# Optimization experiments

Hardware: AMD Instinct MI355X
Metric: run time of the kernel (lower is better)

Reference implementation:

```python
import jax, jax.numpy as jnp
import numpy as np

N, IN_C, HID, H1, E, EP = 4096, 256, 128, 4, 131072, 131072
TH, TL, FF = 4, 2, 512  # transformer heads, layers, ffn dim
D = HID  # transformer d_model


def setup_inputs() -> dict:
    key = jax.random.key(0)
    ks = jax.random.split(key, 32)
    s = 0.05
    inp = {
        'features': jax.random.normal(ks[0], (N, IN_C), jnp.float32),
        'src': jax.random.randint(ks[1], (E,), 0, N),
        'dst': jax.random.randint(ks[2], (E,), 0, N),
        'psrc': jax.random.randint(ks[3], (EP,), 0, N),
        'pdst': jax.random.randint(ks[4], (EP,), 0, N),
        # GAT layer 1: in=256 -> heads=4, out=128
        'W1': jax.random.normal(ks[5], (H1 * HID, IN_C), jnp.float32) * s,
        'al1': jax.random.normal(ks[6], (H1, HID), jnp.float32) * s,
        'ar1': jax.random.normal(ks[7], (H1, HID), jnp.float32) * s,
        'b1': jnp.zeros((H1 * HID,), jnp.float32),
        # GAT layer 2: in=512 -> heads=1, out=128
        'W2': jax.random.normal(ks[8], (HID, H1 * HID), jnp.float32) * s,
        'al2': jax.random.normal(ks[9], (1, HID), jnp.float32) * s,
        'ar2': jax.random.normal(ks[10], (1, HID), jnp.float32) * s,
        'b2': jnp.zeros((HID,), jnp.float32),
        # Transformer encoder (TL layers, torch TransformerEncoderLayer post-norm, relu)
        'tw_qkv': jax.random.normal(ks[11], (TL, 3 * D, D), jnp.float32) * s,
        'tb_qkv': jnp.zeros((TL, 3 * D), jnp.float32),
        'tw_o': jax.random.normal(ks[12], (TL, D, D), jnp.float32) * s,
        'tb_o': jnp.zeros((TL, D), jnp.float32),
        'ln1_g': jnp.ones((TL, D), jnp.float32),
        'ln1_b': jnp.zeros((TL, D), jnp.float32),
        'tw_ff1': jax.random.normal(ks[13], (TL, FF, D), jnp.float32) * s,
        'tb_ff1': jnp.zeros((TL, FF), jnp.float32),
        'tw_ff2': jax.random.normal(ks[14], (TL, D, FF), jnp.float32) * s,
        'tb_ff2': jnp.zeros((TL, D), jnp.float32),
        'ln2_g': jnp.ones((TL, D), jnp.float32),
        'ln2_b': jnp.zeros((TL, D), jnp.float32),
        # decoder MLP
        'fc1_w': jax.random.normal(ks[15], (HID, 2 * HID), jnp.float32) * s,
        'fc1_b': jnp.zeros((HID,), jnp.float32),
        'fc2_w': jax.random.normal(ks[16], (1, HID), jnp.float32) * s,
        'fc2_b': jnp.zeros((1,), jnp.float32),
    }
    return inp


def _leaky(x):
    return jnp.where(x > 0, x, 0.2 * x)


def _gat(x, W, al, ar, b, src, dst, n):
    H, F = al.shape
    h = (x @ W.T).reshape(n, H, F)  # [N,H,F]
    el = jnp.sum(h * al[None], -1)  # [N,H]
    er = jnp.sum(h * ar[None], -1)
    e = _leaky(el[src] + er[dst])  # [E,H]
    m = jax.ops.segment_max(e, dst, num_segments=n)
    ex = jnp.exp(e - m[dst])
    ssum = jax.ops.segment_sum(ex, dst, num_segments=n)
    alpha = ex / ssum[dst]  # edge softmax over incoming edges of dst
    out = jax.ops.segment_sum(h[src] * alpha[:, :, None], dst, num_segments=n)
    return out + b.reshape(1, H, F)


def _ln(x, g, b):
    mu = jnp.mean(x, -1, keepdims=True)
    var = jnp.mean((x - mu) ** 2, -1, keepdims=True)
    return (x - mu) / jnp.sqrt(var + 1e-5) * g + b


def _encoder_layer(h, wqkv, bqkv, wo, bo, g1, b1, wf1, bf1, wf2, bf2, g2, b2):
    n, d = h.shape
    hd = d // TH
    qkv = h @ wqkv.T + bqkv
    q, k, v = jnp.split(qkv, 3, axis=-1)
    q = q.reshape(n, TH, hd)
    k = k.reshape(n, TH, hd)
    v = v.reshape(n, TH, hd)
    scores = jnp.einsum('qhd,khd->hqk', q, k) / jnp.sqrt(jnp.float32(hd))
    attn = jax.nn.softmax(scores, axis=-1)
    o = jnp.einsum('hqk,khd->qhd', attn, v).reshape(n, d) @ wo.T + bo
    h = _ln(h + o, g1, b1)
    ff = jax.nn.relu(h @ wf1.T + bf1) @ wf2.T + bf2
    return _ln(h + ff, g2, b2)


def reference(features, W1, al1, ar1, b1, W2, al2, ar2, b2,
              tw_qkv, tb_qkv, tw_o, tb_o, ln1_g, ln1_b,
              tw_ff1, tb_ff1, tw_ff2, tb_ff2, ln2_g, ln2_b,
              fc1_w, fc1_b, fc2_w, fc2_b, src, dst, psrc, pdst):
    n = features.shape[0]
    h = _gat(features, W1, al1, ar1, b1, src, dst, n)  # [N,4,128]
    h = jax.nn.relu(h.reshape(n, -1))                  # [N,512]
    h = _gat(h, W2, al2, ar2, b2, src, dst, n)[:, 0]   # [N,128]
    for i in range(TL):
        h = _encoder_layer(h, tw_qkv[i], tb_qkv[i], tw_o[i], tb_o[i],
                           ln1_g[i], ln1_b[i], tw_ff1[i], tb_ff1[i],
                           tw_ff2[i], tb_ff2[i], ln2_g[i], ln2_b[i])
    ef = jnp.concatenate([h[psrc], h[pdst]], axis=1)   # [EP,256]
    x = jax.nn.relu(ef @ fc1_w.T + fc1_b)
    return jax.nn.sigmoid(x @ fc2_w.T + fc2_b)         # [EP,1]
```

## Files before the change

kernel.cpp:

```cpp
#include <hip/hip_runtime.h>
#include <hip/hip_bf16.h>
#include <math.h>

#define NN   4096
#define INC  256
#define HIDF 128
#define H1H  4
#define DM   128
#define THD  4
#define FFD  512

typedef __attribute__((ext_vector_type(8))) short bf16x8;
typedef __attribute__((ext_vector_type(4))) float f32x4;

__device__ __forceinline__ float leaky(float x){ return x > 0.f ? x : 0.2f*x; }

__device__ __forceinline__ ushort f2b(float f){
  __hip_bfloat16 h = __float2bfloat16(f);
  return __builtin_bit_cast(ushort, h);
}
__device__ __forceinline__ unsigned pk2(float a, float b){
  return (unsigned)f2b(a) | ((unsigned)f2b(b) << 16);
}
__device__ __forceinline__ float b2f(unsigned u){ return __uint_as_float(u << 16); }
__device__ __forceinline__ float b2flo(unsigned u){ return __uint_as_float(u << 16); }
__device__ __forceinline__ float b2fhi(unsigned u){ return __uint_as_float(u & 0xffff0000u); }

__device__ __forceinline__ int kvperm(int kv){
  return (kv & ~31) | ((kv & 12) << 1) | ((kv >> 2) & 4) | (kv & 3);
}

template<bool BIAS, bool RELU, bool OUTBF, bool ABF>
__global__ __launch_bounds__(256) void gemm_mf(
    const void* __restrict__ Av, const ushort* __restrict__ Wb,
    const float* __restrict__ bias, void* __restrict__ Cv,
    int M, int N, int K, int ldw)
{
  __shared__ uint4 As4[512];
  __shared__ uint4 Bs4[512];
  int tid = threadIdx.x;
  int row0 = blockIdx.y * 64, col0 = blockIdx.x * 64;
  int wid = tid >> 6, lane = tid & 63;
  int wm = wid >> 1, wn = wid & 1;
  int ql = lane & 15, g = lane >> 4;
  const f32x4 z4 = {0.f,0.f,0.f,0.f};
  f32x4 acc[2][2] = {z4,z4,z4,z4};

  for (int k0 = 0; k0 < K; k0 += 64) {
    #pragma unroll
    for (int p = 0; p < 2; p++) {
      int idx = tid + p*256;
      int ko = idx & 7, mm = idx >> 3;
      if constexpr (ABF) {
        As4[ko*64 + mm] = *(const uint4*)((const ushort*)Av + (size_t)(row0 + mm)*K + k0 + ko*8);
      } else {
        const float* sa = (const float*)Av + (size_t)(row0 + mm)*K + k0 + ko*8;
        float4 a0 = *(const float4*)sa;
        float4 a1 = *(const float4*)(sa + 4);
        uint4 av;
        av.x = pk2(a0.x, a0.y); av.y = pk2(a0.z, a0.w);
        av.z = pk2(a1.x, a1.y); av.w = pk2(a1.z, a1.w);
        As4[ko*64 + mm] = av;
      }
      Bs4[ko*64 + mm] = *(const uint4*)(Wb + (size_t)(col0 + mm)*ldw + k0 + ko*8);
    }
    __syncthreads();
    #pragma unroll
    for (int kk = 0; kk < 2; kk++) {
      int ko = kk*4 + g;
      bf16x8 a0 = *((const bf16x8*)As4 + ko*64 + wm*32 + ql);
      bf16x8 a1 = *((const bf16x8*)As4 + ko*64 + wm*32 + 16 + ql);
      bf16x8 b0 = *((const bf16x8*)Bs4 + ko*64 + wn*32 + ql);
      bf16x8 b1 = *((const bf16x8*)Bs4 + ko*64 + wn*32 + 16 + ql);
      acc[0][0] = __builtin_amdgcn_mfma_f32_16x16x32_bf16(a0, b0, acc[0][0], 0,0,0);
      acc[0][1] = __builtin_amdgcn_mfma_f32_16x16x32_bf16(a0, b1, acc[0][1], 0,0,0);
      acc[1][0] = __builtin_amdgcn_mfma_f32_16x16x32_bf16(a1, b0, acc[1][0], 0,0,0);
      acc[1][1] = __builtin_amdgcn_mfma_f32_16x16x32_bf16(a1, b1, acc[1][1], 0,0,0);
    }
    __syncthreads();
  }
  float bvs[2] = {0.f, 0.f};
  if (BIAS) {
    bvs[0] = bias[col0 + wn*32 + ql];
    bvs[1] = bias[col0 + wn*32 + 16 + ql];
  }
  #pragma unroll
  for (int fm = 0; fm < 2; fm++)
    #pragma unroll
    for (int fn = 0; fn < 2; fn++) {
      int row = row0 + wm*32 + fm*16 + g*4;
      int col = col0 + wn*32 + fn*16 + ql;
      #pragma unroll
      for (int r = 0; r < 4; r++) {
        float v = acc[fm][fn][r];
        if (BIAS) v += bvs[fn];
        if (RELU) v = fmaxf(v, 0.f);
        if (OUTBF) ((ushort*)Cv)[(size_t)(row + r)*N + col] = f2b(v);
        else       ((float*)Cv)[(size_t)(row + r)*N + col] = v;
      }
    }
}

__global__ __launch_bounds__(256) void gemm_qkv(
    const ushort* __restrict__ Ab, const ushort* __restrict__ Wb,
    const float* __restrict__ bias,
    ushort* __restrict__ qb, ushort* __restrict__ kt, ushort* __restrict__ vt)
{
  __shared__ uint4 As4[512];
  __shared__ uint4 Bs4[512];
  int tid = threadIdx.x;
  int row0 = blockIdx.y * 64, col0 = blockIdx.x * 64;
  int wid = tid >> 6, lane = tid & 63;
  int wm = wid >> 1, wn = wid & 1;
  int ql = lane & 15, g = lane >> 4;
  const f32x4 z4 = {0.f,0.f,0.f,0.f};
  f32x4 acc[2][2] = {z4,z4,z4,z4};

  for (int k0 = 0; k0 < 128; k0 += 64) {
    #pragma unroll
    for (int p = 0; p < 2; p++) {
      int idx = tid + p*256;
      int ko = idx & 7, mm = idx >> 3;
      As4[ko*64 + mm] = *(const uint4*)(Ab + (size_t)(row0 + mm)*128 + k0 + ko*8);
      Bs4[ko*64 + mm] = *(const uint4*)(Wb + (size_t)(col0 + mm)*128 + k0 + ko*8);
    }
    __syncthreads();
    #pragma unroll
    for (int kk = 0; kk < 2; kk++) {
      int ko = kk*4 + g;
      bf16x8 a0 = *((const bf16x8*)As4 + ko*64 + wm*32 + ql);
      bf16x8 a1 = *((const bf16x8*)As4 + ko*64 + wm*32 + 16 + ql);
      bf16x8 b0 = *((const bf16x8*)Bs4 + ko*64 + wn*32 + ql);
      bf16x8 b1 = *((const bf16x8*)Bs4 + ko*64 + wn*32 + 16 + ql);
      acc[0][0] = __builtin_amdgcn_mfma_f32_16x16x32_bf16(a0, b0, acc[0][0], 0,0,0);
      acc[0][1] = __builtin_amdgcn_mfma_f32_16x16x32_bf16(a0, b1, acc[0][1], 0,0,0);
      acc[1][0] = __builtin_amdgcn_mfma_f32_16x16x32_bf16(a1, b0, acc[1][0], 0,0,0);
      acc[1][1] = __builtin_amdgcn_mfma_f32_16x16x32_bf16(a1, b1, acc[1][1], 0,0,0);
    }
    __syncthreads();
  }
  float bvs[2];
  bvs[0] = bias[col0 + wn*32 + ql];
  bvs[1] = bias[col0 + wn*32 + 16 + ql];
  #pragma unroll
  for (int fm = 0; fm < 2; fm++)
    #pragma unroll
    for (int fn = 0; fn < 2; fn++) {
      int row = row0 + wm*32 + fm*16 + g*4;
      int col = col0 + wn*32 + fn*16 + ql;
      #pragma unroll
      for (int r = 0; r < 4; r++) {
        float v = acc[fm][fn][r] + bvs[fn];
        int kv = row + r;
        if (col < 128) {
          qb[(size_t)kv*128 + col] = f2b(v * 0.25505654708f);
        } else if (col < 256) {
          int hh = (col - 128) >> 5, d = (col - 128) & 31;
          kt[(size_t)hh*131072 + (size_t)kv*32 + d] = f2b(v);
        } else {
          int hh = (col - 256) >> 5, d = (col - 256) & 31;
          vt[(size_t)hh*131072 + (size_t)(kv >> 5)*1024 + (d >> 4)*512
             + (d & 15)*32 + kvperm(kv & 31)] = f2b(v);
        }
      }
    }
}

template<bool DEC>
__global__ __launch_bounds__(256) void gemm_ln(
    const ushort* __restrict__ Ab, const ushort* __restrict__ Wb,
    const float* __restrict__ bias, ushort* __restrict__ h,
    const float* __restrict__ lng, const float* __restrict__ lnb, int K,
    const ushort* __restrict__ Wdec, const float* __restrict__ bias256,
    ushort* __restrict__ ABp)
{
  __shared__ uint4 As4[128];
  __shared__ uint4 Bs4[1024];
  __shared__ float xs[16][132];
  __shared__ ushort xsb[16][136];
  int tid = threadIdx.x;
  int row0 = blockIdx.x * 16;
  int wv = tid >> 6, lane = tid & 63;
  int ql = lane & 15, g = lane >> 4;
  const f32x4 z4 = {0.f,0.f,0.f,0.f};
  f32x4 acc[2] = {z4, z4};

  for (int k0 = 0; k0 < K; k0 += 64) {
    if (tid < 128) {
      int ko = tid & 7, mm = tid >> 3;
      As4[ko*16 + mm] = *(const uint4*)(Ab + (size_t)(row0 + mm)*K + k0 + ko*8);
    }
    #pragma unroll
    for (int p = 0; p < 4; p++) {
      int idx = tid + p*256;
      int ko = idx & 7, nn = idx >> 3;
      Bs4[ko*128 + nn] = *(const uint4*)(Wb + (size_t)nn*K + k0 + ko*8);
    }
    __syncthreads();
    #pragma unroll
    for (int kk = 0; kk < 2; kk++) {
      int ko = kk*4 + g;
      bf16x8 a = *((const bf16x8*)As4 + ko*16 + ql);
      #pragma unroll
      for (int fn = 0; fn < 2; fn++) {
        bf16x8 b = *((const bf16x8*)Bs4 + ko*128 + wv*32 + fn*16 + ql);
        acc[fn] = __builtin_amdgcn_mfma_f32_16x16x32_bf16(a, b, acc[fn], 0,0,0);
      }
    }
    __syncthreads();
  }
  #pragma unroll
  for (int fn = 0; fn < 2; fn++) {
    int col = wv*32 + fn*16 + ql;
    float bv = bias[col];
    #pragma unroll
    for (int r = 0; r < 4; r++) xs[g*4 + r][col] = acc[fn][r] + bv;
  }
  __syncthreads();
  int rl = tid >> 4, cl = tid & 15, c0 = cl * 8;
  ushort* hrow = h + (size_t)(row0 + rl)*128;
  uint4 rv = *(const uint4*)(hrow + c0);
  float x[8];
  x[0] = xs[rl][c0+0] + b2flo(rv.x); x[1] = xs[rl][c0+1] + b2fhi(rv.x);
  x[2] = xs[rl][c0+2] + b2flo(rv.y); x[3] = xs[rl][c0+3] + b2fhi(rv.y);
  x[4] = xs[rl][c0+4] + b2flo(rv.z); x[5] = xs[rl][c0+5] + b2fhi(rv.z);
  x[6] = xs[rl][c0+6] + b2flo(rv.w); x[7] = xs[rl][c0+7] + b2fhi(rv.w);
  float s1 = 0.f, s2 = 0.f;
  #pragma unroll
  for (int i = 0; i < 8; i++) { s1 += x[i]; s2 += x[i]*x[i]; }
  #pragma unroll
  for (int st = 1; st < 16; st <<= 1) {
    s1 += __shfl_xor(s1, st); s2 += __shfl_xor(s2, st);
  }
  float mean = s1 * (1.f/128.f);
  float var  = s2 * (1.f/128.f) - mean*mean;
  float rstd = rsqrtf(var + 1e-5f);
  float o[8];
  #pragma unroll
  for (int i = 0; i < 8; i += 4) {
    float4 g4 = *(const float4*)(lng + c0 + i);
    float4 b4 = *(const float4*)(lnb + c0 + i);
    o[i+0] = (x[i+0]-mean)*rstd*g4.x + b4.x;
    o[i+1] = (x[i+1]-mean)*rstd*g4.y + b4.y;
    o[i+2] = (x[i+2]-mean)*rstd*g4.z + b4.z;
    o[i+3] = (x[i+3]-mean)*rstd*g4.w + b4.w;
  }
  uint4 ov; ov.x = pk2(o[0],o[1]); ov.y = pk2(o[2],o[3]);
  ov.z = pk2(o[4],o[5]); ov.w = pk2(o[6],o[7]);
  if constexpr (!DEC) {
    *(uint4*)(hrow + c0) = ov;
  } else {
    *(uint4*)(&xsb[rl][c0]) = ov;
    __syncthreads();
    f32x4 acc2[4] = {z4, z4, z4, z4};
    for (int kk = 0; kk < 4; kk++) {
      #pragma unroll
      for (int p = 0; p < 4; p++) {
        int idx = tid + p*256;
        int ko = idx & 3, row = idx >> 2;
        Bs4[ko*256 + (row ^ (ko << 2))] =
            *(const uint4*)(Wdec + (size_t)row*128 + kk*32 + ko*8);
      }
      __syncthreads();
      bf16x8 a = *(const bf16x8*)(&xsb[ql][kk*32 + g*8]);
      #pragma unroll
      for (int fn = 0; fn < 4; fn++) {
        int col = wv*64 + fn*16 + ql;
        bf16x8 b = *((const bf16x8*)Bs4 + g*256 + (col ^ (g << 2)));
        acc2[fn] = __builtin_amdgcn_mfma_f32_16x16x32_bf16(a, b, acc2[fn], 0,0,0);
      }
      __syncthreads();
    }
    #pragma unroll
    for (int fn = 0; fn < 4; fn++) {
      int col = wv*64 + fn*16 + ql;
      float bv = bias256[col];
      #pragma unroll
      for (int r = 0; r < 4; r++)
        ABp[(size_t)(row0 + g*4 + r)*256 + col] = f2b(acc2[fn][r] + bv);
    }
  }
}

__global__ __launch_bounds__(256) void gemm_hg_elr(
    const ushort* __restrict__ Ab, const ushort* __restrict__ Wb,
    const float* __restrict__ al, const float* __restrict__ ar,
    ushort* __restrict__ hg, float* __restrict__ el, float* __restrict__ er)
{
  __shared__ uint4 As4[128];
  __shared__ uint4 Bs4[1024];
  __shared__ float xs[16][132];
  int tid = threadIdx.x;
  int row0 = blockIdx.x * 16;
  int wv = tid >> 6, lane = tid & 63;
  int ql = lane & 15, g = lane >> 4;
  const f32x4 z4 = {0.f,0.f,0.f,0.f};
  f32x4 acc[2] = {z4, z4};

  for (int k0 = 0; k0 < 512; k0 += 64) {
    if (tid < 128) {
      int ko = tid & 7, mm = tid >> 3;
      As4[ko*16 + mm] = *(const uint4*)(Ab + (size_t)(row0 + mm)*512 + k0 + ko*8);
    }
    #pragma unroll
    for (int p = 0; p < 4; p++) {
      int idx = tid + p*256;
      int ko = idx & 7, nn = idx >> 3;
      Bs4[ko*128 + nn] = *(const uint4*)(Wb + (size_t)nn*512 + k0 + ko*8);
    }
    __syncthreads();
    #pragma unroll
    for (int kk = 0; kk < 2; kk++) {
      int ko = kk*4 + g;
      bf16x8 a = *((const bf16x8*)As4 + ko*16 + ql);
      #pragma unroll
      for (int fn = 0; fn < 2; fn++) {
        bf16x8 b = *((const bf16x8*)Bs4 + ko*128 + wv*32 + fn*16 + ql);
        acc[fn] = __builtin_amdgcn_mfma_f32_16x16x32_bf16(a, b, acc[fn], 0,0,0);
      }
    }
    __syncthreads();
  }
  #pragma unroll
  for (int fn = 0; fn < 2; fn++) {
    int col = wv*32 + fn*16 + ql;
    #pragma unroll
    for (int r = 0; r < 4; r++) xs[g*4 + r][col] = acc[fn][r];
  }
  __syncthreads();
  int rl = tid >> 4, cl = tid & 15, c0 = cl * 8;
  float e1 = 0.f, e2 = 0.f;
  float x[8];
  #pragma unroll
  for (int i = 0; i < 8; i += 4) {
    float4 a4 = *(const float4*)(al + c0 + i);
    float4 r4 = *(const float4*)(ar + c0 + i);
    x[i+0] = xs[rl][c0+i+0]; x[i+1] = xs[rl][c0+i+1];
    x[i+2] = xs[rl][c0+i+2]; x[i+3] = xs[rl][c0+i+3];
    e1 += x[i+0]*a4.x + x[i+1]*a4.y + x[i+2]*a4.z + x[i+3]*a4.w;
    e2 += x[i+0]*r4.x + x[i+1]*r4.y + x[i+2]*r4.z + x[i+3]*r4.w;
  }
  uint4 ov; ov.x = pk2(x[0],x[1]); ov.y = pk2(x[2],x[3]);
  ov.z = pk2(x[4],x[5]); ov.w = pk2(x[6],x[7]);
  *(uint4*)(hg + (size_t)(row0 + rl)*128 + c0) = ov;
  #pragma unroll
  for (int st = 1; st < 16; st <<= 1) {
    e1 += __shfl_xor(e1, st); e2 += __shfl_xor(e2, st);
  }
  if (cl == 0) { el[row0 + rl] = e1; er[row0 + rl] = e2; }
}

__global__ __launch_bounds__(256) void cvt_all(
    const float* __restrict__ W1, const float* __restrict__ W2,
    const float* __restrict__ qkv, const float* __restrict__ o,
    const float* __restrict__ ff1, const float* __restrict__ ff2,
    const float* __restrict__ fc1, const float* __restrict__ fc1b,
    const float* __restrict__ feat,
    ushort* __restrict__ out, float* __restrict__ bias256,
    ushort* __restrict__ featb,
    const int* __restrict__ dst, int* __restrict__ deg, int E)
{
  int b = blockIdx.x;
  if (b >= 1633) {
    int e = (b - 1633)*256 + threadIdx.x;
    if (e < E) atomicAdd(&deg[dst[e]], 1);
    return;
  }
  if (b == 608) {
    int t = threadIdx.x;
    bias256[t] = (t < 128) ? fc1b[t] : 0.f;
    return;
  }
  if (b >= 609) {
    int i = ((b - 609)*256 + threadIdx.x) * 4;
    float4 v = *(const float4*)(feat + i);
    uint2 w; w.x = pk2(v.x, v.y); w.y = pk2(v.z, v.w);
    *(uint2*)(featb + i) = w;
    return;
  }
  int i4 = (b*256 + threadIdx.x) * 4;
  const float* s; int loc;
  size_t dstoff = i4;
  if      (i4 < 131072) { s = W1;  loc = i4; }
  else if (i4 < 196608) { s = W2;  loc = i4 - 131072; }
  else if (i4 < 294912) { s = qkv; loc = i4 - 196608; }
  else if (i4 < 327680) { s = o;   loc = i4 - 294912; }
  else if (i4 < 458752) { s = ff1; loc = i4 - 327680; }
  else if (i4 < 589824) { s = ff2; loc = i4 - 458752; }
  else {
    s = fc1; loc = i4 - 589824;
    int j = loc >> 8, k2 = loc & 255;
    dstoff = 589824 + ((k2 >= 128) ? 16384 : 0) + j*128 + (k2 & 127);
  }
  float4 v = *(const float4*)(s + loc);
  uint2 w; w.x = pk2(v.x, v.y); w.y = pk2(v.z, v.w);
  *(uint2*)(out + dstoff) = w;
}

__global__ __launch_bounds__(1024) void scan_kernel(
    const int* __restrict__ deg, int* __restrict__ rowstart, int* __restrict__ cursor)
{
  __shared__ int sdata[1024];
  int t = threadIdx.x;
  int base = t * 4;
  int v0 = deg[base], v1 = deg[base+1], v2 = deg[base+2], v3 = deg[base+3];
  int tot = v0 + v1 + v2 + v3;
  sdata[t] = tot;
  __syncthreads();
  for (int off = 1; off < 1024; off <<= 1) {
    int x = (t >= off) ? sdata[t - off] : 0;
    __syncthreads();
    sdata[t] += x;
    __syncthreads();
  }
  int run = sdata[t] - tot;
  rowstart[base]   = run; cursor[base]   = run; run += v0;
  rowstart[base+1] = run; cursor[base+1] = run; run += v1;
  rowstart[base+2] = run; cursor[base+2] = run; run += v2;
  rowstart[base+3] = run; cursor[base+3] = run; run += v3;
  if (t == 1023) rowstart[4096] = run;
}
__global__ void fill_kernel(const int* __restrict__ src, const int* __restrict__ dst,
                            int* __restrict__ cursor, int* __restrict__ nbr, int E) {
  int e = blockIdx.x * blockDim.x + threadIdx.x;
  if (e < E) {
    int p = atomicAdd(&cursor[dst[e]], 1);
    nbr[p] = src[e];
  }
}

__global__ __launch_bounds__(256) void elr4_kernel(
    const ushort* __restrict__ hmat, const float* __restrict__ al,
    const float* __restrict__ ar, float* __restrict__ el, float* __restrict__ er)
{
  int w = threadIdx.x >> 6, lane = threadIdx.x & 63;
  int n = blockIdx.x * 4 + w;
  int hh = lane >> 4, f0 = (lane & 15) * 8;
  bf16x8 hv = *(const bf16x8*)(hmat + (size_t)n*512 + hh*128 + f0);
  float4 a0 = *(const float4*)(al + hh*128 + f0);
  float4 a1 = *(const float4*)(al + hh*128 + f0 + 4);
  float4 r0 = *(const float4*)(ar + hh*128 + f0);
  float4 r1 = *(const float4*)(ar + hh*128 + f0 + 4);
  float x[8];
  #pragma unroll
  for (int i = 0; i < 8; i++) x[i] = b2f((ushort)hv[i]);
  float e1 = x[0]*a0.x + x[1]*a0.y + x[2]*a0.z + x[3]*a0.w
           + x[4]*a1.x + x[5]*a1.y + x[6]*a1.z + x[7]*a1.w;
  float e2 = x[0]*r0.x + x[1]*r0.y + x[2]*r0.z + x[3]*r0.w
           + x[4]*r1.x + x[5]*r1.y + x[6]*r1.z + x[7]*r1.w;
  #pragma unroll
  for (int s = 1; s < 16; s <<= 1) { e1 += __shfl_xor(e1, s); e2 += __shfl_xor(e2, s); }
  if ((lane & 15) == 0) { el[n*4 + hh] = e1; er[n*4 + hh] = e2; }
}

__global__ __launch_bounds__(256) void gat_agg4(
    const ushort* __restrict__ hsrc, const float* __restrict__ el, const float* __restrict__ er,
    const int* __restrict__ rowstart, const int* __restrict__ nbr,
    const float* __restrict__ bias, ushort* __restrict__ out)
{
  __shared__ float s_alpha[4][256][4];
  __shared__ int   s_nbr[4][256];
  int wv = threadIdx.x >> 6, lane = threadIdx.x & 63;
  int n = blockIdx.x * 4 + wv;
  int e0 = rowstart[n];
  int deg = rowstart[n+1] - e0;
  float4 ern = *(const float4*)(er + (size_t)n*4);
  int hh = lane >> 4;
  float acc[8] = {};
  if (deg > 0 && deg <= 256) {
    float se0=0.f, se1=0.f, se2=0.f, se3=0.f;
    for (int i = lane; i < deg; i += 64) {
      int s = nbr[e0 + i];
      s_nbr[wv][i] = s;
      float4 ev = *(const float4*)(el + (size_t)s*4);
      float p0 = __expf(leaky(ev.x + ern.x));
      float p1 = __expf(leaky(ev.y + ern.y));
      float p2 = __expf(leaky(ev.z + ern.z));
      float p3 = __expf(leaky(ev.w + ern.w));
      s_alpha[wv][i][0] = p0; s_alpha[wv][i][1] = p1;
      s_alpha[wv][i][2] = p2; s_alpha[wv][i][3] = p3;
      se0 += p0; se1 += p1; se2 += p2; se3 += p3;
    }
    #pragma unroll
    for (int st = 1; st < 64; st <<= 1) {
      se0 += __shfl_xor(se0, st); se1 += __shfl_xor(se1, st);
      se2 += __shfl_xor(se2, st); se3 += __shfl_xor(se3, st);
    }
    float si = 1.f / ((hh == 0) ? se0 : (hh == 1) ? se1 : (hh == 2) ? se2 : se3);
    #pragma unroll 4
    for (int i = 0; i < deg; i++) {
      float a = s_alpha[wv][i][hh] * si;
      int s = s_nbr[wv][i];
      uint4 hv = *(const uint4*)(hsrc + (size_t)s*512 + lane*8);
      acc[0] += a * b2flo(hv.x); acc[1] += a * b2fhi(hv.x);
      acc[2] += a * b2flo(hv.y); acc[3] += a * b2fhi(hv.y);
      acc[4] += a * b2flo(hv.z); acc[5] += a * b2fhi(hv.z);
      acc[6] += a * b2flo(hv.w); acc[7] += a * b2fhi(hv.w);
    }
  } else if (deg > 0) {
    float se0=0.f, se1=0.f, se2=0.f, se3=0.f;
    for (int i = lane; i < deg; i += 64) {
      int s = nbr[e0 + i];
      float4 ev = *(const float4*)(el + (size_t)s*4);
      se0 += __expf(leaky(ev.x + ern.x));
      se1 += __expf(leaky(ev.y + ern.y));
      se2 += __expf(leaky(ev.z + ern.z));
      se3 += __expf(leaky(ev.w + ern.w));
    }
    #pragma unroll
    for (int st = 1; st < 64; st <<= 1) {
      se0 += __shfl_xor(se0, st); se1 += __shfl_xor(se1, st);
      se2 += __shfl_xor(se2, st); se3 += __shfl_xor(se3, st);
    }
    float si0 = 1.f/se0, si1 = 1.f/se1, si2 = 1.f/se2, si3 = 1.f/se3;
    for (int c = 0; c < deg; c += 256) {
      int cn = min(256, deg - c);
      for (int i = lane; i < cn; i += 64) {
        int s = nbr[e0 + c + i];
        s_nbr[wv][i] = s;
        float4 ev = *(const float4*)(el + (size_t)s*4);
        s_alpha[wv][i][0] = __expf(leaky(ev.x + ern.x)) * si0;
        s_alpha[wv][i][1] = __expf(leaky(ev.y + ern.y)) * si1;
        s_alpha[wv][i][2] = __expf(leaky(ev.z + ern.z)) * si2;
        s_alpha[wv][i][3] = __expf(leaky(ev.w + ern.w)) * si3;
      }
      #pragma unroll 4
      for (int i = 0; i < cn; i++) {
        float a = s_alpha[wv][i][hh];
        int s = s_nbr[wv][i];
        uint4 hv = *(const uint4*)(hsrc + (size_t)s*512 + lane*8);
        acc[0] += a * b2flo(hv.x); acc[1] += a * b2fhi(hv.x);
        acc[2] += a * b2flo(hv.y); acc[3] += a * b2fhi(hv.y);
        acc[4] += a * b2flo(hv.z); acc[5] += a * b2fhi(hv.z);
        acc[6] += a * b2flo(hv.w); acc[7] += a * b2fhi(hv.w);
      }
    }
  }
  const float* bp = bias + lane*8;
  float4 b0 = *(const float4*)(bp);
  float4 b1 = *(const float4*)(bp + 4);
  float v0 = fmaxf(acc[0]+b0.x, 0.f), v1 = fmaxf(acc[1]+b0.y, 0.f);
  float v2 = fmaxf(acc[2]+b0.z, 0.f), v3 = fmaxf(acc[3]+b0.w, 0.f);
  float v4 = fmaxf(acc[4]+b1.x, 0.f), v5 = fmaxf(acc[5]+b1.y, 0.f);
  float v6 = fmaxf(acc[6]+b1.z, 0.f), v7 = fmaxf(acc[7]+b1.w, 0.f);
  uint4 ov; ov.x = pk2(v0,v1); ov.y = pk2(v2,v3); ov.z = pk2(v4,v5); ov.w = pk2(v6,v7);
  *(uint4*)(out + (size_t)n*512 + lane*8) = ov;
}

__global__ __launch_bounds__(256) void gat_agg1(
    const ushort* __restrict__ hsrc, const float* __restrict__ el, const float* __restrict__ er,
    const int* __restrict__ rowstart, const int* __restrict__ nbr,
    const float* __restrict__ bias, ushort* __restrict__ out)
{
  __shared__ float s_alpha[4][256];
  __shared__ int   s_nbr[4][256];
  int wv = threadIdx.x >> 6, lane = threadIdx.x & 63;
  int n = blockIdx.x * 4 + wv;
  int e0 = rowstart[n];
  int deg = rowstart[n+1] - e0;
  float ern = er[n];
  float a0 = 0.f, a1 = 0.f;
  if (deg > 0 && deg <= 256) {
    float se = 0.f;
    for (int i = lane; i < deg; i += 64) {
      int s = nbr[e0 + i];
      s_nbr[wv][i] = s;
      float p = __expf(leaky(el[s] + ern));
      s_alpha[wv][i] = p;
      se += p;
    }
    #pragma unroll
    for (int st = 1; st < 64; st <<= 1) se += __shfl_xor(se, st);
    float si = 1.f / se;
    #pragma unroll 4
    for (int i = 0; i < deg; i++) {
      float a = s_alpha[wv][i] * si;
      int s = s_nbr[wv][i];
      unsigned u = *(const unsigned*)(hsrc + (size_t)s*128 + lane*2);
      a0 += a * b2flo(u);
      a1 += a * b2fhi(u);
    }
  } else if (deg > 0) {
    float se = 0.f;
    for (int i = lane; i < deg; i += 64)
      se += __expf(leaky(el[nbr[e0 + i]] + ern));
    #pragma unroll
    for (int st = 1; st < 64; st <<= 1) se += __shfl_xor(se, st);
    float si = 1.f / se;
    for (int c = 0; c < deg; c += 256) {
      int cn = min(256, deg - c);
      for (int i = lane; i < cn; i += 64) {
        int s = nbr[e0 + c + i];
        s_nbr[wv][i] = s;
        s_alpha[wv][i] = __expf(leaky(el[s] + ern)) * si;
      }
      #pragma unroll 4
      for (int i = 0; i < cn; i++) {
        float a = s_alpha[wv][i];
        int s = s_nbr[wv][i];
        unsigned u = *(const unsigned*)(hsrc + (size_t)s*128 + lane*2);
        a0 += a * b2flo(u);
        a1 += a * b2fhi(u);
      }
    }
  }
  float v0 = a0 + bias[lane*2], v1 = a1 + bias[lane*2 + 1];
  *(unsigned*)(out + (size_t)n*128 + lane*2) = pk2(v0, v1);
}

#define LOADFRAGS(KF, VF, KV)                                              \
  {                                                                        \
    int _kv = (KV);                                                        \
    if (_kv < 512) {                                                       \
      const ushort* _kp = kptr + (size_t)_kv * 32;                         \
      const ushort* _vp = vptr + (size_t)_kv * 32;                         \
      KF[0] = *(const bf16x8*)(_kp);                                       \
      KF[1] = *(const bf16x8*)(_kp + 512);                                 \
      KF[2] = *(const bf16x8*)(_kp + 1024);                                \
      KF[3] = *(const bf16x8*)(_kp + 1536);                                \
      VF[0] = *(const bf16x8*)(_vp);                                       \
      VF[1] = *(const bf16x8*)(_vp + 1024);                                \
      VF[2] = *(const bf16x8*)(_vp + 512);                                 \
      VF[3] = *(const bf16x8*)(_vp + 1536);                                \
    }                                                                      \
  }

#define QPASS(QF, LS, OA, OB, KF, VF)                                      \
  {                                                                        \
    f32x4 st0 = __builtin_amdgcn_mfma_f32_16x16x32_bf16(KF[0], QF, z4, 0, 0, 0); \
    f32x4 st1 = __builtin_amdgcn_mfma_f32_16x16x32_bf16(KF[1], QF, z4, 0, 0, 0); \
    f32x4 st2 = __builtin_amdgcn_mfma_f32_16x16x32_bf16(KF[2], QF, z4, 0, 0, 0); \
    f32x4 st3 = __builtin_amdgcn_mfma_f32_16x16x32_bf16(KF[3], QF, z4, 0, 0, 0); \
    float pvv[16];                                                         \
    _Pragma("unroll")                                                      \
    for (int i = 0; i < 4; i++) {                                          \
      pvv[i] = st0[i]; pvv[4+i] = st1[i]; pvv[8+i] = st2[i]; pvv[12+i] = st3[i]; \
    }                                                                      \
    _Pragma("unroll")                                                      \
    for (int i = 0; i < 16; i++) { pvv[i] = exp2f(pvv[i]); LS += pvv[i]; } \
    bf16x8 pf0 = { (short)f2b(pvv[0]),  (short)f2b(pvv[1]),  (short)f2b(pvv[2]),  (short)f2b(pvv[3]),   \
                   (short)f2b(pvv[4]),  (short)f2b(pvv[5]),  (short)f2b(pvv[6]),  (short)f2b(pvv[7]) }; \
    bf16x8 pf1 = { (short)f2b(pvv[8]),  (short)f2b(pvv[9]),  (short)f2b(pvv[10]), (short)f2b(pvv[11]),  \
                   (short)f2b(pvv[12]), (short)f2b(pvv[13]), (short)f2b(pvv[14]), (short)f2b(pvv[15]) };\
    OA = __builtin_amdgcn_mfma_f32_16x16x32_bf16(VF[0], pf0, OA, 0, 0, 0); \
    OA = __builtin_amdgcn_mfma_f32_16x16x32_bf16(VF[1], pf1, OA, 0, 0, 0); \
    OB = __builtin_amdgcn_mfma_f32_16x16x32_bf16(VF[2], pf0, OB, 0, 0, 0); \
    OB = __builtin_amdgcn_mfma_f32_16x16x32_bf16(VF[3], pf1, OB, 0, 0, 0); \
  }

#define ATTN_BODY(KF, VF, KN, VN, KV)                                      \
  {                                                                        \
    LOADFRAGS(KN, VN, (KV) + 64);                                          \
    QPASS(qf0, ls0, o00, o01, KF, VF);                                     \
    QPASS(qf1, ls1, o10, o11, KF, VF);                                     \
  }

__global__ __launch_bounds__(512) void attn_mfma(
    const ushort* __restrict__ qb,
    const ushort* __restrict__ kt,
    const ushort* __restrict__ vt,
    ushort* __restrict__ attnout)
{
  int lane = threadIdx.x & 63;
  int w    = threadIdx.x >> 6;
  int head = blockIdx.x >> 7;
  int q0   = (blockIdx.x & 127) * 32;
  int ql = lane & 15;
  int g  = lane >> 4;
  const f32x4 z4 = {0.f, 0.f, 0.f, 0.f};
  int kvbase = w * 512;

  bf16x8 qf0 = *(const bf16x8*)(qb + (size_t)(q0 + ql)*128      + head*32 + g*8);
  bf16x8 qf1 = *(const bf16x8*)(qb + (size_t)(q0 + 16 + ql)*128 + head*32 + g*8);
  const ushort* kptr = kt + (size_t)head*131072 + (size_t)kvbase*32 + ql*32 + g*8;
  const ushort* vptr = vt + (size_t)head*131072 + (size_t)kvbase*32 + ql*32 + g*8;

  float ls0 = 0.f, ls1 = 0.f;
  f32x4 o00 = z4, o01 = z4, o10 = z4, o11 = z4;

  bf16x8 kfA[4], vfA[4], kfB[4], vfB[4];
  LOADFRAGS(kfA, vfA, 0);
  for (int kv0 = 0; kv0 < 512; kv0 += 128) {
    ATTN_BODY(kfA, vfA, kfB, vfB, kv0);
    ATTN_BODY(kfB, vfB, kfA, vfA, kv0 + 64);
  }

  ls0 += __shfl_xor(ls0, 16); ls0 += __shfl_xor(ls0, 32);
  ls1 += __shfl_xor(ls1, 16); ls1 += __shfl_xor(ls1, 32);

  __shared__ float so[8][32][36];
  __shared__ float sl[8][32];
  if (g == 0) { sl[w][ql] = ls0; sl[w][16 + ql] = ls1; }
  #pragma unroll
  for (int r = 0; r < 4; r++) {
    so[w][ql][g*4 + r]           = o00[r];
    so[w][ql][16 + g*4 + r]      = o01[r];
    so[w][16 + ql][g*4 + r]      = o10[r];
    so[w][16 + ql][16 + g*4 + r] = o11[r];
  }
  __syncthreads();
  int q  = threadIdx.x >> 4;
  int d0 = (threadIdx.x & 15) * 2;
  float L = 0.f, O0 = 0.f, O1 = 0.f;
  #pragma unroll
  for (int w2 = 0; w2 < 8; w2++) {
    L  += sl[w2][q];
    O0 += so[w2][q][d0];
    O1 += so[w2][q][d0+1];
  }
  float rl = 1.f / L;
  *(unsigned*)(attnout + (size_t)(q0 + q)*128 + head*32 + d0) = pk2(O0*rl, O1*rl);
}

__global__ __launch_bounds__(256) void pair_kernel(
    const ushort* __restrict__ ABp,
    const int* __restrict__ ps, const int* __restrict__ pd,
    const float* __restrict__ fc2w, const float* __restrict__ fc2b,
    float* __restrict__ out, int EP)
{
  int gw = (blockIdx.x * blockDim.x + threadIdx.x) >> 6;
  int lane = threadIdx.x & 63;
  int nw = (gridDim.x * blockDim.x) >> 6;
  float w0 = fc2w[2*lane], w1 = fc2w[2*lane + 1];
  float bb = fc2b[0];
  for (int p = gw*4; p < EP; p += nw*4) {
    float acc[4];
    #pragma unroll
    for (int k = 0; k < 4; k++) {
      int pp = (p + k < EP) ? (p + k) : (EP - 1);
      int s = ps[pp], d = pd[pp];
      unsigned av = *(const unsigned*)(ABp + (size_t)s*256 + 2*lane);
      unsigned bv = *(const unsigned*)(ABp + (size_t)d*256 + 128 + 2*lane);
      acc[k] = fmaxf(b2flo(av) + b2flo(bv), 0.f)*w0
             + fmaxf(b2fhi(av) + b2fhi(bv), 0.f)*w1;
    }
    #pragma unroll
    for (int off = 32; off > 0; off >>= 1) {
      #pragma unroll
      for (int k = 0; k < 4; k++) acc[k] += __shfl_down(acc[k], off);
    }
    if (lane == 0) {
      #pragma unroll
      for (int k = 0; k < 4; k++)
        if (p + k < EP) out[p + k] = 1.f / (1.f + __expf(-(acc[k] + bb)));
    }
  }
}

extern "C" void kernel_launch(void* const* d_in, const int* in_sizes, int n_in,
                              void* d_out, int out_size, void* d_ws, size_t ws_size,
                              hipStream_t stream)
{
  const float* features = (const float*)d_in[0];
  const int*   src      = (const int*)d_in[1];
  const int*   dst      = (const int*)d_in[2];
  const int*   psrc     = (const int*)d_in[3];
  const int*   pdst     = (const int*)d_in[4];
  const float* W1   = (const float*)d_in[5];
  const float* al1  = (const float*)d_in[6];
  const float* ar1  = (const float*)d_in[7];
  const float* b1   = (const float*)d_in[8];
  const float* W2   = (const float*)d_in[9];
  const float* al2  = (const float*)d_in[10];
  const float* ar2  = (const float*)d_in[11];
  const float* b2   = (const float*)d_in[12];
  const float* tw_qkv = (const float*)d_in[13];
  const float* tb_qkv = (const float*)d_in[14];
  const float* tw_o   = (const float*)d_in[15];
  const float* tb_o   = (const float*)d_in[16];
  const float* ln1_g  = (const float*)d_in[17];
  const float* ln1_b  = (const float*)d_in[18];
  const float* tw_ff1 = (const float*)d_in[19];
  const float* tb_ff1 = (const float*)d_in[20];
  const float* tw_ff2 = (const float*)d_in[21];
  const float* tb_ff2 = (const float*)d_in[22];
  const float* ln2_g  = (const float*)d_in[23];
  const float* ln2_b  = (const float*)d_in[24];
  const float* fc1_w  = (const float*)d_in[25];
  const float* fc1_b  = (const float*)d_in[26];
  const float* fc2_w  = (const float*)d_in[27];
  const float* fc2_b  = (const float*)d_in[28];
  int E  = in_sizes[1];
  int EP = in_sizes[3];

  float* ws = (float*)d_ws;
  size_t off = 0;
  auto alloc = [&](size_t n) { float* p = ws + off; off += n; return p; };
  ushort* hb    = (ushort*)alloc((size_t)NN * 64);
  ushort* featb = (ushort*)alloc((size_t)NN * 128);
  ushort* h1b   = (ushort*)alloc((size_t)NN * 256);
  ushort* h2b   = (ushort*)alloc((size_t)NN * 256);
  ushort* bigb  = (ushort*)alloc((size_t)NN * 256);
  ushort* hgb   = (ushort*)alloc((size_t)NN * 64);
  ushort* qb    = (ushort*)alloc((size_t)NN * 64);
  ushort* attnb = (ushort*)alloc((size_t)NN * 64);
  ushort* kt    = (ushort*)alloc((size_t)NN * 64);
  ushort* vt    = (ushort*)alloc((size_t)NN * 64);
  ushort* wbf   = (ushort*)alloc(622592/2);
  ushort* ABp   = (ushort*)alloc((size_t)NN * 128);
  float*  bias256 = alloc(256);
  float*  el1   = alloc((size_t)NN * 4);
  float*  er1   = alloc((size_t)NN * 4);
  float*  el2   = alloc((size_t)NN);
  float*  er2   = alloc((size_t)NN);
  int* ibase    = (int*)(ws + off);
  int* deg      = ibase;
  int* rowstart = ibase + 4096;
  int* cursor   = rowstart + 4097;
  int* nbr      = cursor + 4096;

  const size_t oW1 = 0, oW2 = 131072, oQKV = 196608, oO = 294912,
               oFF1 = 327680, oFF2 = 458752, oFC1 = 589824;

  hipMemsetAsync(deg, 0, 4096 * sizeof(int), stream);
  cvt_all<<<1633 + 512, 256, 0, stream>>>(W1, W2, tw_qkv, tw_o, tw_ff1, tw_ff2,
                                          fc1_w, fc1_b, features, wbf, bias256,
                                          featb, dst, deg, E);
  scan_kernel<<<1, 1024, 0, stream>>>(deg, rowstart, cursor);
  fill_kernel<<<(E + 255)/256, 256, 0, stream>>>(src, dst, cursor, nbr, E);

  gemm_mf<false,false,true,true><<<dim3(8, 64), 256, 0, stream>>>(
      featb, wbf + oW1, nullptr, h1b, NN, 512, 256, 256);
  elr4_kernel<<<1024, 256, 0, stream>>>(h1b, al1, ar1, el1, er1);
  gat_agg4<<<1024, 256, 0, stream>>>(h1b, el1, er1, rowstart, nbr, b1, h2b);

  gemm_hg_elr<<<256, 256, 0, stream>>>(h2b, wbf + oW2, al2, ar2, hgb, el2, er2);
  gat_agg1<<<1024, 256, 0, stream>>>(hgb, el2, er2, rowstart, nbr, b2, hb);

  for (int l = 0; l < 2; l++) {
    gemm_qkv<<<dim3(6, 64), 256, 0, stream>>>(
        hb, wbf + oQKV + (size_t)l*49152, tb_qkv + l*384, qb, kt, vt);
    attn_mfma<<<512, 512, 0, stream>>>(qb, kt, vt, attnb);
    gemm_ln<false><<<256, 256, 0, stream>>>(
        attnb, wbf + oO + (size_t)l*16384, tb_o + l*128, hb,
        ln1_g + l*128, ln1_b + l*128, 128, nullptr, nullptr, nullptr);
    gemm_mf<true,true,true,true><<<dim3(8, 64), 256, 0, stream>>>(
        hb, wbf + oFF1 + (size_t)l*65536, tb_ff1 + l*512, bigb, NN, 512, 128, 128);
    if (l == 0) {
      gemm_ln<false><<<256, 256, 0, stream>>>(
          bigb, wbf + oFF2 + (size_t)l*65536, tb_ff2 + l*128, hb,
          ln2_g + l*128, ln2_b + l*128, 512, nullptr, nullptr, nullptr);
    } else {
      gemm_ln<true><<<256, 256, 0, stream>>>(
          bigb, wbf + oFF2 + (size_t)l*65536, tb_ff2 + l*128, hb,
          ln2_g + l*128, ln2_b + l*128, 512, wbf + oFC1, bias256, ABp);
    }
  }

  pair_kernel<<<1024, 256, 0, stream>>>(ABp, psrc, pdst, fc2_w, fc2_b, (float*)d_out, EP);
}
```

Baseline: 200.8 us.

## Fuse out-proj+LN, FF1 and FF2+LN into one cooperative kernel with grid syncs

Replaces three separate launches per encoder layer (the output-projection GEMM with LayerNorm, FF1 with ReLU, and FF2 with LayerNorm plus the optional decoder projection) with one cooperative kernel of 512 blocks. The stages are separated by grid.sync() and share one static shared-memory buffer. The goal is to remove launch gaps and per-kernel tail overhead between small dependent GEMMs. In exchange, the GEMM-LN stages leave half the blocks idle, `dec` becomes a runtime branch instead of a template parameter, and grid barriers add their own cost.

```diff
diff --git a/kernel.cpp b/kernel.cpp
--- a/kernel.cpp
+++ b/kernel.cpp
@@ -1,6 +1,9 @@
 #include <hip/hip_runtime.h>
 #include <hip/hip_bf16.h>
+#include <hip/hip_cooperative_groups.h>
 #include <math.h>
+
+namespace cg = cooperative_groups;
 
 #define NN   4096
 #define INC  256
@@ -166,20 +169,20 @@
     }
 }
 
-template<bool DEC>
-__global__ __launch_bounds__(256) void gemm_ln(
+__device__ void dev_gemm_ln(
+    int b, char* smem,
     const ushort* __restrict__ Ab, const ushort* __restrict__ Wb,
     const float* __restrict__ bias, ushort* __restrict__ h,
     const float* __restrict__ lng, const float* __restrict__ lnb, int K,
     const ushort* __restrict__ Wdec, const float* __restrict__ bias256,
-    ushort* __restrict__ ABp)
-{
-  __shared__ uint4 As4[128];
-  __shared__ uint4 Bs4[1024];
-  __shared__ float xs[16][132];
-  __shared__ ushort xsb[16][136];
+    ushort* __restrict__ ABp, int dec)
+{
+  uint4* As4 = (uint4*)smem;
+  uint4* Bs4 = (uint4*)(smem + 2048);
+  float (*xs)[132] = (float(*)[132])(smem + 18432);
+  ushort (*xsb)[136] = (ushort(*)[136])(smem + 26880);
   int tid = threadIdx.x;
-  int row0 = blockIdx.x * 16;
+  int row0 = b * 16;
   int wv = tid >> 6, lane = tid & 63;
   int ql = lane & 15, g = lane >> 4;
   const f32x4 z4 = {0.f,0.f,0.f,0.f};
@@ -203,8 +206,8 @@
       bf16x8 a = *((const bf16x8*)As4 + ko*16 + ql);
       #pragma unroll
       for (int fn = 0; fn < 2; fn++) {
-        bf16x8 b = *((const bf16x8*)Bs4 + ko*128 + wv*32 + fn*16 + ql);
-        acc[fn] = __builtin_amdgcn_mfma_f32_16x16x32_bf16(a, b, acc[fn], 0,0,0);
+        bf16x8 bb = *((const bf16x8*)Bs4 + ko*128 + wv*32 + fn*16 + ql);
+        acc[fn] = __builtin_amdgcn_mfma_f32_16x16x32_bf16(a, bb, acc[fn], 0,0,0);
       }
     }
     __syncthreads();
@@ -247,7 +250,7 @@
   }
   uint4 ov; ov.x = pk2(o[0],o[1]); ov.y = pk2(o[2],o[3]);
   ov.z = pk2(o[4],o[5]); ov.w = pk2(o[6],o[7]);
-  if constexpr (!DEC) {
+  if (!dec) {
     *(uint4*)(hrow + c0) = ov;
   } else {
     *(uint4*)(&xsb[rl][c0]) = ov;
@@ -266,8 +269,8 @@
       #pragma unroll
       for (int fn = 0; fn < 4; fn++) {
         int col = wv*64 + fn*16 + ql;
-        bf16x8 b = *((const bf16x8*)Bs4 + g*256 + (col ^ (g << 2)));
-        acc2[fn] = __builtin_amdgcn_mfma_f32_16x16x32_bf16(a, b, acc2[fn], 0,0,0);
+        bf16x8 bb = *((const bf16x8*)Bs4 + g*256 + (col ^ (g << 2)));
+        acc2[fn] = __builtin_amdgcn_mfma_f32_16x16x32_bf16(a, bb, acc2[fn], 0,0,0);
       }
       __syncthreads();
     }
@@ -280,6 +283,84 @@
         ABp[(size_t)(row0 + g*4 + r)*256 + col] = f2b(acc2[fn][r] + bv);
     }
   }
+}
+
+__device__ void dev_ff1(
+    int b, char* smem,
+    const ushort* __restrict__ Ab, const ushort* __restrict__ Wb,
+    const float* __restrict__ bias, ushort* __restrict__ C)
+{
+  uint4* As4 = (uint4*)smem;
+  uint4* Bs4 = (uint4*)(smem + 8192);
+  int tid = threadIdx.x;
+  int row0 = (b >> 3) * 64, col0 = (b & 7) * 64;
+  int wid = tid >> 6, lane = tid & 63;
+  int wm = wid >> 1, wn = wid & 1;
+  int ql = lane & 15, g = lane >> 4;
+  const f32x4 z4 = {0.f,0.f,0.f,0.f};
+  f32x4 acc[2][2] = {z4,z4,z4,z4};
+
+  for (int k0 = 0; k0 < 128; k0 += 64) {
+    #pragma unroll
+    for (int p = 0; p < 2; p++) {
+      int idx = tid + p*256;
+      int ko = idx & 7, mm = idx >> 3;
+      As4[ko*64 + mm] = *(const uint4*)(Ab + (size_t)(row0 + mm)*128 + k0 + ko*8);
+      Bs4[ko*64 + mm] = *(const uint4*)(Wb + (size_t)(col0 + mm)*128 + k0 + ko*8);
+    }
+    __syncthreads();
+    #pragma unroll
+    for (int kk = 0; kk < 2; kk++) {
+      int ko = kk*4 + g;
+      bf16x8 a0 = *((const bf16x8*)As4 + ko*64 + wm*32 + ql);
+      bf16x8 a1 = *((const bf16x8*)As4 + ko*64 + wm*32 + 16 + ql);
+      bf16x8 b0 = *((const bf16x8*)Bs4 + ko*64 + wn*32 + ql);
+      bf16x8 b1 = *((const bf16x8*)Bs4 + ko*64 + wn*32 + 16 + ql);
+      acc[0][0] = __builtin_amdgcn_mfma_f32_16x16x32_bf16(a0, b0, acc[0][0], 0,0,0);
+      acc[0][1] = __builtin_amdgcn_mfma_f32_16x16x32_bf16(a0, b1, acc[0][1], 0,0,0);
+      acc[1][0] = __builtin_amdgcn_mfma_f32_16x16x32_bf16(a1, b0, acc[1][0], 0,0,0);
+      acc[1][1] = __builtin_amdgcn_mfma_f32_16x16x32_bf16(a1, b1, acc[1][1], 0,0,0);
+    }
+    __syncthreads();
+  }
+  float bvs[2];
+  bvs[0] = bias[col0 + wn*32 + ql];
+  bvs[1] = bias[col0 + wn*32 + 16 + ql];
+  #pragma unroll
+  for (int fm = 0; fm < 2; fm++)
+    #pragma unroll
+    for (int fn = 0; fn < 2; fn++) {
+      int row = row0 + wm*32 + fm*16 + g*4;
+      int col = col0 + wn*32 + fn*16 + ql;
+      #pragma unroll
+      for (int r = 0; r < 4; r++) {
+        float v = fmaxf(acc[fm][fn][r] + bvs[fn], 0.f);
+        C[(size_t)(row + r)*512 + col] = f2b(v);
+      }
+    }
+}
+
+__global__ __launch_bounds__(256) void enc_ffn(
+    const ushort* attnb, const ushort* Wo, const float* bo, ushort* hb,
+    const float* ln1g, const float* ln1b,
+    const ushort* Wf1, const float* bf1, ushort* bigb,
+    const ushort* Wf2, const float* bf2,
+    const float* ln2g, const float* ln2b,
+    const ushort* Wdec, const float* bias256, ushort* ABp, int dec)
+{
+  __shared__ uint4 smemU[1952];
+  char* smem = (char*)smemU;
+  cg::grid_group grid = cg::this_grid();
+  int b = blockIdx.x;
+  if (b < 256)
+    dev_gemm_ln(b, smem, attnb, Wo, bo, hb, ln1g, ln1b, 128,
+                nullptr, nullptr, nullptr, 0);
+  grid.sync();
+  dev_ff1(b, smem, hb, Wf1, bf1, bigb);
+  grid.sync();
+  if (b < 256)
+    dev_gemm_ln(b, smem, bigb, Wf2, bf2, hb, ln2g, ln2b, 512,
+                Wdec, bias256, ABp, dec);
 }
 
 __global__ __launch_bounds__(256) void gemm_hg_elr(
@@ -831,20 +912,27 @@
     gemm_qkv<<<dim3(6, 64), 256, 0, stream>>>(
         hb, wbf + oQKV + (size_t)l*49152, tb_qkv + l*384, qb, kt, vt);
     attn_mfma<<<512, 512, 0, stream>>>(qb, kt, vt, attnb);
-    gemm_ln<false><<<256, 256, 0, stream>>>(
-        attnb, wbf + oO + (size_t)l*16384, tb_o + l*128, hb,
-        ln1_g + l*128, ln1_b + l*128, 128, nullptr, nullptr, nullptr);
-    gemm_mf<true,true,true,true><<<dim3(8, 64), 256, 0, stream>>>(
-        hb, wbf + oFF1 + (size_t)l*65536, tb_ff1 + l*512, bigb, NN, 512, 128, 128);
-    if (l == 0) {
-      gemm_ln<false><<<256, 256, 0, stream>>>(
-          bigb, wbf + oFF2 + (size_t)l*65536, tb_ff2 + l*128, hb,
-          ln2_g + l*128, ln2_b + l*128, 512, nullptr, nullptr, nullptr);
-    } else {
-      gemm_ln<true><<<256, 256, 0, stream>>>(
-          bigb, wbf + oFF2 + (size_t)l*65536, tb_ff2 + l*128, hb,
-          ln2_g + l*128, ln2_b + l*128, 512, wbf + oFC1, bias256, ABp);
-    }
+
+    const ushort* Ab_  = attnb;
+    const ushort* Wo_  = wbf + oO + (size_t)l*16384;
+    const float*  bo_  = tb_o + l*128;
+    ushort*       hbp_ = hb;
+    const float*  g1_  = ln1_g + l*128;
+    const float*  b1p_ = ln1_b + l*128;
+    const ushort* Wf1_ = wbf + oFF1 + (size_t)l*65536;
+    const float*  bf1_ = tb_ff1 + l*512;
+    ushort*       big_ = bigb;
+    const ushort* Wf2_ = wbf + oFF2 + (size_t)l*65536;
+    const float*  bf2_ = tb_ff2 + l*128;
+    const float*  g2_  = ln2_g + l*128;
+    const float*  b2p_ = ln2_b + l*128;
+    const ushort* Wd_  = wbf + oFC1;
+    const float*  bs_  = bias256;
+    ushort*       ab_  = ABp;
+    int           dec_ = (l == 1);
+    void* kargs[] = {&Ab_, &Wo_, &bo_, &hbp_, &g1_, &b1p_, &Wf1_, &bf1_, &big_,
+                     &Wf2_, &bf2_, &g2_, &b2p_, &Wd_, &bs_, &ab_, &dec_};
+    hipLaunchCooperativeKernel((void*)enc_ffn, dim3(512), dim3(256), kargs, 0, stream);
   }
 
   pair_kernel<<<1024, 256, 0, stream>>>(ABp, psrc, pdst, fc2_w, fc2_b, (float*)d_out, EP);
```

New measurement: 461.5 us. 2.3x slower.
